# Kernel optimization log

Hardware: AMD Instinct MI355X
Metric: run time of the kernel (lower is better)

## Reference

```python
import jax, jax.numpy as jnp
import numpy as np

BEAM = 64
RANK = 32
VOCAB = 21128


def setup_inputs() -> dict:
    key = jax.random.key(0)
    k1, k2, k3, k4 = jax.random.split(key, 4)
    B, S, V = 16, 256, VOCAB
    emissions = jax.random.normal(k1, (B, S, V), jnp.float32)
    targets = jax.random.randint(k2, (B, S), 0, V)
    mask = jnp.ones((B, S), dtype=bool)
    E1 = jax.random.normal(k3, (V, RANK), jnp.float32) * 0.02
    E2 = jax.random.normal(k4, (V, RANK), jnp.float32) * 0.02
    return {"emissions": emissions, "targets": targets, "mask": mask, "E1": E1, "E2": E2}


def _crf_llh(emissions, targets, mask, E1, E2, beam=BEAM):
    B, S, V = emissions.shape
    maskf = mask.astype(emissions.dtype)

    # ---- numerator: score of the target path ----
    em = jnp.take_along_axis(emissions, targets[:, :, None], axis=2)[:, :, 0]  # [B,S]
    trans = jnp.sum(E1[targets[:, :-1]] * E2[targets[:, 1:]], axis=2)          # [B,S-1]
    scores = em.at[:, 1:].add(trans)
    numerator = jnp.sum(scores * maskf, axis=1)                                # [B]

    # ---- denominator: beam-approximated normalizer ----
    # force target token into the beam (scatter +inf, then topk indices)
    b_idx = jnp.arange(B)[:, None]
    s_idx = jnp.arange(S)[None, :]
    _em = emissions.at[b_idx, s_idx, targets].set(jnp.inf)
    _, beam_targets = jax.lax.top_k(_em, beam)                                 # [B,S,beam]
    beam_em = jnp.take_along_axis(emissions, beam_targets, axis=2)             # [B,S,beam]

    t1 = E1[beam_targets[:, :-1]]                                              # [B,S-1,beam,rank]
    t2 = E2[beam_targets[:, 1:]]                                               # [B,S-1,beam,rank]
    beam_trans = jnp.einsum('bsir,bsjr->bsij', t1, t2)                         # [B,S-1,beam,beam]

    score0 = beam_em[:, 0]                                                     # [B,beam]

    def step(score, x):
        trans_i, emit_i, m_i = x
        nxt = jax.scipy.special.logsumexp(score[:, :, None] + trans_i, axis=1) + emit_i
        score = jnp.where(m_i[:, None], nxt, score)
        return score, None

    xs = (jnp.swapaxes(beam_trans, 0, 1),          # [S-1,B,beam,beam]
          jnp.swapaxes(beam_em[:, 1:], 0, 1),      # [S-1,B,beam]
          jnp.swapaxes(mask[:, 1:], 0, 1))         # [S-1,B]
    score, _ = jax.lax.scan(step, score0, xs)
    denominator = jax.scipy.special.logsumexp(score, axis=1)                   # [B]

    llh = numerator - denominator
    return jnp.sum(llh)  # reduction='sum'


def reference(emissions, targets, mask, E1, E2):
    return _crf_llh(emissions, targets, mask, E1, E2)
```

## Files before the change

kernel.cpp:

```cpp
#include <hip/hip_runtime.h>
#include <stdint.h>

#define Bn 16
#define Sn 256
#define Vn 21128
#define NV4 5282
#define RANKn 32
#define BEAMn 64
#define HBINS 4096
#define CAPn 512
#define LOG2E 1.44269504088896340736f
#define LN2   0.69314718055994530942f

#define EXP2F(x) __builtin_amdgcn_exp2f(x)
#define LOG2F(x) __builtin_amdgcn_logf(x)

__device__ __forceinline__ unsigned f2o(unsigned b) {
    return (b & 0x80000000u) ? ~b : (b | 0x80000000u);
}
__device__ __forceinline__ float o2f(unsigned u) {
    unsigned b = (u & 0x80000000u) ? (u ^ 0x80000000u) : ~u;
    return __uint_as_float(b);
}
__device__ __forceinline__ float rdlane(float v, int lane) {
    return __int_as_float(__builtin_amdgcn_readlane(__float_as_int(v), lane));
}

__global__ __launch_bounds__(256) void topk_kernel(const float* __restrict__ emis,
                                                   const int* __restrict__ targets,
                                                   int* __restrict__ beam_idx,
                                                   float* __restrict__ beam_val) {
    const int row = blockIdx.x;
    const float* __restrict__ rowp = emis + (size_t)row * Vn;
    const int tgt = targets[row];
    __shared__ unsigned hist[HBINS];
    __shared__ unsigned csum[256];
    __shared__ unsigned cu[CAPn];
    __shared__ int      cix[CAPn];
    __shared__ int      selidx[BEAMn];
    __shared__ float    selval[BEAMn];
    __shared__ unsigned ccount;
    __shared__ int      binstar;
    __shared__ int      chunkc;
    __shared__ int      hastgt;
    const int t = threadIdx.x;
    for (int i = t; i < HBINS; i += 256) hist[i] = 0;
    if (t == 0) { ccount = 0; hastgt = 0; }
    __syncthreads();
    uint4 vals[21];
    #pragma unroll
    for (int it = 0; it < 21; ++it) {
        int v4 = t + it * 256;
        if (v4 < NV4) {
            const uint4 raw = ((const uint4*)rowp)[v4];
            uint4 u;
            u.x = f2o(raw.x); u.y = f2o(raw.y); u.z = f2o(raw.z); u.w = f2o(raw.w);
            vals[it] = u;
            atomicAdd(&hist[u.x >> 20], 1u);
            atomicAdd(&hist[u.y >> 20], 1u);
            atomicAdd(&hist[u.z >> 20], 1u);
            atomicAdd(&hist[u.w >> 20], 1u);
        }
    }
    __syncthreads();
    unsigned cs = 0;
    #pragma unroll
    for (int i = 0; i < 16; ++i) cs += hist[t * 16 + i];
    csum[t] = cs;
    __syncthreads();
    for (int off = 1; off < 256; off <<= 1) {
        unsigned v = csum[t] + ((t + off < 256) ? csum[t + off] : 0u);
        __syncthreads();
        csum[t] = v;
        __syncthreads();
    }
    if (csum[t] >= BEAMn && (t == 255 || csum[t + 1] < BEAMn)) chunkc = t;
    __syncthreads();
    if (t == 0) {
        int tc = chunkc;
        unsigned acc = (tc == 255) ? 0u : csum[tc + 1];
        int bs = tc * 16;
        for (int b2 = tc * 16 + 15; b2 >= tc * 16; --b2) {
            acc += hist[b2];
            if (acc >= BEAMn) { bs = b2; break; }
        }
        binstar = bs;
    }
    __syncthreads();
    const unsigned bstar = (unsigned)binstar;
    #pragma unroll
    for (int it = 0; it < 21; ++it) {
        int v4 = t + it * 256;
        if (v4 < NV4) {
            uint4 u = vals[it];
            int bi = v4 * 4;
            if ((u.x >> 20) >= bstar) { unsigned p = atomicAdd(&ccount, 1u); if (p < CAPn) { cu[p] = u.x; cix[p] = bi;     } }
            if ((u.y >> 20) >= bstar) { unsigned p = atomicAdd(&ccount, 1u); if (p < CAPn) { cu[p] = u.y; cix[p] = bi + 1; } }
            if ((u.z >> 20) >= bstar) { unsigned p = atomicAdd(&ccount, 1u); if (p < CAPn) { cu[p] = u.z; cix[p] = bi + 2; } }
            if ((u.w >> 20) >= bstar) { unsigned p = atomicAdd(&ccount, 1u); if (p < CAPn) { cu[p] = u.w; cix[p] = bi + 3; } }
        }
    }
    __syncthreads();
    const int C = (int)min(ccount, (unsigned)CAPn);
    for (int p = t; p < C; p += 256) {
        unsigned up = cu[p]; int ip = cix[p];
        int rank = 0;
        for (int q = 0; q < C; ++q) {
            unsigned uq = cu[q];
            rank += (uq > up) || (uq == up && cix[q] < ip);
        }
        if (rank < BEAMn) { selidx[rank] = ip; selval[rank] = o2f(up); }
    }
    __syncthreads();
    if (t < BEAMn && selidx[t] == tgt) hastgt = 1;
    __syncthreads();
    if (t == 0 && !hastgt) { selidx[BEAMn - 1] = tgt; selval[BEAMn - 1] = rowp[tgt]; }
    __syncthreads();
    if (t < BEAMn) {
        beam_idx[(size_t)row * BEAMn + t] = selidx[t];
        beam_val[(size_t)row * BEAMn + t] = selval[t];
    }
}

#define TPAD 68
__global__ __launch_bounds__(256) void trans_kernel(const float* __restrict__ E1,
                                                    const float* __restrict__ E2,
                                                    const int* __restrict__ beam_idx,
                                                    float* __restrict__ trans) {
    const int blk = blockIdx.x;
    const int b = blk / (Sn - 1);
    const int k = blk - b * (Sn - 1);
    const int* bi = beam_idx + ((size_t)(b * Sn + k)) * BEAMn;
    const int* bj = beam_idx + ((size_t)(b * Sn + k + 1)) * BEAMn;
    __shared__ float e1t[RANKn][TPAD];
    __shared__ float e2t[RANKn][TPAD];
    const int t = threadIdx.x;
    {
        const int row = t >> 2, q = t & 3;
        const int rb = q * 8;
        int i1 = bi[row];
        const float4* s1 = (const float4*)(E1 + (size_t)i1 * RANKn) + q * 2;
        float4 a0 = s1[0], a1 = s1[1];
        e1t[rb + 0][row] = a0.x; e1t[rb + 1][row] = a0.y; e1t[rb + 2][row] = a0.z; e1t[rb + 3][row] = a0.w;
        e1t[rb + 4][row] = a1.x; e1t[rb + 5][row] = a1.y; e1t[rb + 6][row] = a1.z; e1t[rb + 7][row] = a1.w;
        int i2 = bj[row];
        const float4* s2 = (const float4*)(E2 + (size_t)i2 * RANKn) + q * 2;
        float4 b0 = s2[0], b1 = s2[1];
        e2t[rb + 0][row] = b0.x; e2t[rb + 1][row] = b0.y; e2t[rb + 2][row] = b0.z; e2t[rb + 3][row] = b0.w;
        e2t[rb + 4][row] = b1.x; e2t[rb + 5][row] = b1.y; e2t[rb + 6][row] = b1.z; e2t[rb + 7][row] = b1.w;
    }
    __syncthreads();
    const int ti = t & 15, tj = t >> 4;
    const int i0 = ti * 4, j0 = tj * 4;
    float acc[4][4] = {};
    #pragma unroll
    for (int r = 0; r < RANKn; ++r) {
        float4 a = *(const float4*)&e1t[r][i0];
        float4 bb = *(const float4*)&e2t[r][j0];
        acc[0][0] += a.x * bb.x; acc[0][1] += a.x * bb.y; acc[0][2] += a.x * bb.z; acc[0][3] += a.x * bb.w;
        acc[1][0] += a.y * bb.x; acc[1][1] += a.y * bb.y; acc[1][2] += a.y * bb.z; acc[1][3] += a.y * bb.w;
        acc[2][0] += a.z * bb.x; acc[2][1] += a.z * bb.y; acc[2][2] += a.z * bb.z; acc[2][3] += a.z * bb.w;
        acc[3][0] += a.w * bb.x; acc[3][1] += a.w * bb.y; acc[3][2] += a.w * bb.z; acc[3][3] += a.w * bb.w;
    }
    float* outp = trans + (size_t)blk * (BEAMn * BEAMn);
    #pragma unroll
    for (int ii = 0; ii < 4; ++ii) {
        float4 o = { EXP2F(acc[ii][0] * LOG2E), EXP2F(acc[ii][1] * LOG2E),
                     EXP2F(acc[ii][2] * LOG2E), EXP2F(acc[ii][3] * LOG2E) };
        *(float4*)&outp[(i0 + ii) * BEAMn + j0] = o;
    }
}

__global__ __launch_bounds__(512) void scan_kernel(const float* __restrict__ trans,
                                                   const float* __restrict__ beam_val,
                                                   const int* __restrict__ mask,
                                                   float* __restrict__ out) {
    const int b = blockIdx.x;
    const int t = threadIdx.x;
    const int c = t >> 6, j = t & 63;
    const float* __restrict__ trb = trans + (size_t)b * (Sn - 1) * (BEAMn * BEAMn);
    const float* __restrict__ bv  = beam_val + (size_t)b * Sn * BEAMn;
    const int* __restrict__ mk = mask + (size_t)b * Sn;
    __shared__ float psum[2][8][BEAMn + 1];

    const unsigned long long mb0 = __ballot(mk[j] != 0);
    const unsigned long long mb1 = __ballot(mk[64 + j] != 0);
    const unsigned long long mb2 = __ballot(mk[128 + j] != 0);
    const unsigned long long mb3 = __ballot(mk[192 + j] != 0);

    float score_reg = bv[j] * LOG2E;
    float tba[8], tbb[8], tbc[8];
    float eba, ebb, ebc;
    const float* tp0 = trb + (c * 8) * BEAMn + j;
    #pragma unroll
    for (int r = 0; r < 8; ++r) tba[r] = tp0[r * BEAMn];
    #pragma unroll
    for (int r = 0; r < 8; ++r) tbb[r] = tp0[4096 + r * BEAMn];
    eba = bv[BEAMn + j] * LOG2E;
    ebb = bv[2 * BEAMn + j] * LOG2E;
    ebc = 0.f;

#define SSTEP(K, TA, EA, TC, EC)  {                                           \
    if ((K) + 2 < Sn - 1) {                                                   \
        const float* tpn = tp0 + (size_t)((K) + 2) * 4096;                    \
        _Pragma("unroll")                                                     \
        for (int r = 0; r < 8; ++r) TC[r] = tpn[r * BEAMn];                   \
        EC = bv[(size_t)((K) + 3) * BEAMn + j] * LOG2E;                       \
    }                                                                         \
    const float mt = rdlane(score_reg, 0);                                    \
    const float pj = EXP2F(score_reg - mt);                                   \
    float acc;                                                                \
    acc  = rdlane(pj, c * 8 + 0) * TA[0];                                     \
    acc += rdlane(pj, c * 8 + 1) * TA[1];                                     \
    acc += rdlane(pj, c * 8 + 2) * TA[2];                                     \
    acc += rdlane(pj, c * 8 + 3) * TA[3];                                     \
    acc += rdlane(pj, c * 8 + 4) * TA[4];                                     \
    acc += rdlane(pj, c * 8 + 5) * TA[5];                                     \
    acc += rdlane(pj, c * 8 + 6) * TA[6];                                     \
    acc += rdlane(pj, c * 8 + 7) * TA[7];                                     \
    psum[(K) & 1][c][j] = acc;                                                \
    __asm__ volatile("s_waitcnt lgkmcnt(0)\n\ts_barrier" ::: "memory");       \
    {                                                                         \
        const float (*ps)[BEAMn + 1] = psum[(K) & 1];                         \
        float tot = ps[0][j] + ps[1][j] + ps[2][j] + ps[3][j]                 \
                  + ps[4][j] + ps[5][j] + ps[6][j] + ps[7][j];                \
        float nxt = mt + LOG2F(tot) + EA;                                     \
        const int kk1 = (K) + 1;                                              \
        const unsigned long long bsel =                                       \
            (kk1 < 64) ? mb0 : (kk1 < 128) ? mb1 : (kk1 < 192) ? mb2 : mb3;  \
        score_reg = ((bsel >> (kk1 & 63)) & 1ull) ? nxt : score_reg;          \
    }                                                                         \
}

    for (int kb = 0; kb < Sn - 1; kb += 3) {
        SSTEP(kb,     tba, eba, tbc, ebc);
        SSTEP(kb + 1, tbb, ebb, tba, eba);
        SSTEP(kb + 2, tbc, ebc, tbb, ebb);
    }
#undef SSTEP

    if (t < BEAMn) {
        float v = score_reg;
        for (int off = 32; off; off >>= 1) v = fmaxf(v, __shfl_xor(v, off, 64));
        float e = EXP2F(score_reg - v);
        for (int off = 32; off; off >>= 1) e += __shfl_xor(e, off, 64);
        if (t == 0) atomicAdd(out, -LN2 * (v + LOG2F(e)));
    }
}

__global__ __launch_bounds__(256) void num_kernel(const float* __restrict__ emis,
                                                  const int* __restrict__ targets,
                                                  const int* __restrict__ mask,
                                                  const float* __restrict__ E1,
                                                  const float* __restrict__ E2,
                                                  float* __restrict__ out) {
    const int gid = blockIdx.x * 256 + threadIdx.x;
    float val = 0.f;
    if (gid < Bn * Sn) {
        int s = gid & (Sn - 1);
        int tg = targets[gid];
        float em = emis[(size_t)gid * Vn + tg];
        float tr = 0.f;
        if (s > 0) {
            int pv = targets[gid - 1];
            const float4* p1 = (const float4*)(E1 + (size_t)pv * RANKn);
            const float4* p2 = (const float4*)(E2 + (size_t)tg * RANKn);
            #pragma unroll
            for (int r = 0; r < 8; ++r) {
                float4 a = p1[r], bb = p2[r];
                tr += a.x * bb.x + a.y * bb.y + a.z * bb.z + a.w * bb.w;
            }
        }
        if (mask[gid]) val = em + tr;
    }
    for (int off = 32; off; off >>= 1) val += __shfl_xor(val, off, 64);
    __shared__ float wsum[4];
    if ((threadIdx.x & 63) == 0) wsum[threadIdx.x >> 6] = val;
    __syncthreads();
    if (threadIdx.x == 0) atomicAdd(out, wsum[0] + wsum[1] + wsum[2] + wsum[3]);
}

extern "C" void kernel_launch(void* const* d_in, const int* in_sizes, int n_in,
                              void* d_out, int out_size, void* d_ws, size_t ws_size,
                              hipStream_t stream) {
    const float* emis    = (const float*)d_in[0];
    const int*   targets = (const int*)d_in[1];
    const int*   mask    = (const int*)d_in[2];
    const float* E1      = (const float*)d_in[3];
    const float* E2      = (const float*)d_in[4];
    float* out = (float*)d_out;
    char* ws = (char*)d_ws;
    int*   beam_idx = (int*)ws;
    float* beam_val = (float*)(ws + (1 << 20));
    float* trans    = (float*)(ws + (2 << 20));

    (void)hipMemsetAsync(out, 0, sizeof(float), stream);
    hipLaunchKernelGGL(topk_kernel, dim3(Bn * Sn), dim3(256), 0, stream,
                       emis, targets, beam_idx, beam_val);
    hipLaunchKernelGGL(trans_kernel, dim3(Bn * (Sn - 1)), dim3(256), 0, stream,
                       E1, E2, beam_idx, trans);
    hipLaunchKernelGGL(num_kernel, dim3((Bn * Sn + 255) / 256), dim3(256), 0, stream,
                       emis, targets, mask, E1, E2, out);
    hipLaunchKernelGGL(scan_kernel, dim3(Bn), dim3(512), 0, stream,
                       trans, beam_val, mask, out);
}
```

Baseline: 679.0 us.

## Parallelize forward scan via segmented matrix products and add threshold fast path for top-k

The sequential 255-step logsumexp scan, which ran on only 16 blocks, is replaced by a segmented approach. 256 blocks each multiply 16 exp-domain transition matrices (with max-normalization tracked as a log scale), and a small finale kernel chains the 16 segment products per batch. Separately, top-k first tries a fixed value threshold (2.5) to collect candidates directly, skipping the histogram and prefix-scan passes when the count lands between 64 and 512, and falls back to the histogram otherwise. This trades far more arithmetic (64x64 matmuls) for much more parallelism, and adds exp-domain precision risk from rescaling by the max.

```diff
diff --git a/kernel.cpp b/kernel.cpp
--- a/kernel.cpp
+++ b/kernel.cpp
@@ -9,6 +9,7 @@
 #define BEAMn 64
 #define HBINS 4096
 #define CAPn 512
+#define NSEG 16
 #define LOG2E 1.44269504088896340736f
 #define LN2   0.69314718055994530942f
 
@@ -22,8 +23,8 @@
     unsigned b = (u & 0x80000000u) ? (u ^ 0x80000000u) : ~u;
     return __uint_as_float(b);
 }
-__device__ __forceinline__ float rdlane(float v, int lane) {
-    return __int_as_float(__builtin_amdgcn_readlane(__float_as_int(v), lane));
+__device__ __forceinline__ float dot4(float4 a, float4 b) {
+    return a.x * b.x + a.y * b.y + a.z * b.z + a.w * b.w;
 }
 
 __global__ __launch_bounds__(256) void topk_kernel(const float* __restrict__ emis,
@@ -43,11 +44,13 @@
     __shared__ int      binstar;
     __shared__ int      chunkc;
     __shared__ int      hastgt;
+    __shared__ unsigned wcnt[4];
     const int t = threadIdx.x;
-    for (int i = t; i < HBINS; i += 256) hist[i] = 0;
     if (t == 0) { ccount = 0; hastgt = 0; }
-    __syncthreads();
+
+    const unsigned THRU = f2o(__float_as_uint(2.5f));
     uint4 vals[21];
+    unsigned cntl = 0;
     #pragma unroll
     for (int it = 0; it < 21; ++it) {
         int v4 = t + it * 256;
@@ -56,48 +59,78 @@
             uint4 u;
             u.x = f2o(raw.x); u.y = f2o(raw.y); u.z = f2o(raw.z); u.w = f2o(raw.w);
             vals[it] = u;
-            atomicAdd(&hist[u.x >> 20], 1u);
-            atomicAdd(&hist[u.y >> 20], 1u);
-            atomicAdd(&hist[u.z >> 20], 1u);
-            atomicAdd(&hist[u.w >> 20], 1u);
-        }
-    }
-    __syncthreads();
-    unsigned cs = 0;
-    #pragma unroll
-    for (int i = 0; i < 16; ++i) cs += hist[t * 16 + i];
-    csum[t] = cs;
-    __syncthreads();
-    for (int off = 1; off < 256; off <<= 1) {
-        unsigned v = csum[t] + ((t + off < 256) ? csum[t + off] : 0u);
-        __syncthreads();
-        csum[t] = v;
-        __syncthreads();
-    }
-    if (csum[t] >= BEAMn && (t == 255 || csum[t + 1] < BEAMn)) chunkc = t;
-    __syncthreads();
-    if (t == 0) {
-        int tc = chunkc;
-        unsigned acc = (tc == 255) ? 0u : csum[tc + 1];
-        int bs = tc * 16;
-        for (int b2 = tc * 16 + 15; b2 >= tc * 16; --b2) {
-            acc += hist[b2];
-            if (acc >= BEAMn) { bs = b2; break; }
-        }
-        binstar = bs;
-    }
-    __syncthreads();
-    const unsigned bstar = (unsigned)binstar;
-    #pragma unroll
-    for (int it = 0; it < 21; ++it) {
-        int v4 = t + it * 256;
-        if (v4 < NV4) {
-            uint4 u = vals[it];
-            int bi = v4 * 4;
-            if ((u.x >> 20) >= bstar) { unsigned p = atomicAdd(&ccount, 1u); if (p < CAPn) { cu[p] = u.x; cix[p] = bi;     } }
-            if ((u.y >> 20) >= bstar) { unsigned p = atomicAdd(&ccount, 1u); if (p < CAPn) { cu[p] = u.y; cix[p] = bi + 1; } }
-            if ((u.z >> 20) >= bstar) { unsigned p = atomicAdd(&ccount, 1u); if (p < CAPn) { cu[p] = u.z; cix[p] = bi + 2; } }
-            if ((u.w >> 20) >= bstar) { unsigned p = atomicAdd(&ccount, 1u); if (p < CAPn) { cu[p] = u.w; cix[p] = bi + 3; } }
+            cntl += (u.x > THRU) + (u.y > THRU) + (u.z > THRU) + (u.w > THRU);
+        }
+    }
+    for (int off = 32; off; off >>= 1) cntl += __shfl_xor(cntl, off, 64);
+    if ((t & 63) == 0) wcnt[t >> 6] = cntl;
+    __syncthreads();
+    const unsigned C0 = wcnt[0] + wcnt[1] + wcnt[2] + wcnt[3];
+
+    if (C0 >= BEAMn && C0 <= CAPn) {
+        #pragma unroll
+        for (int it = 0; it < 21; ++it) {
+            int v4 = t + it * 256;
+            if (v4 < NV4) {
+                uint4 u = vals[it];
+                int bi = v4 * 4;
+                if (u.x > THRU) { unsigned p = atomicAdd(&ccount, 1u); cu[p] = u.x; cix[p] = bi;     }
+                if (u.y > THRU) { unsigned p = atomicAdd(&ccount, 1u); cu[p] = u.y; cix[p] = bi + 1; }
+                if (u.z > THRU) { unsigned p = atomicAdd(&ccount, 1u); cu[p] = u.z; cix[p] = bi + 2; }
+                if (u.w > THRU) { unsigned p = atomicAdd(&ccount, 1u); cu[p] = u.w; cix[p] = bi + 3; }
+            }
+        }
+    } else {
+        for (int i = t; i < HBINS; i += 256) hist[i] = 0;
+        __syncthreads();
+        #pragma unroll
+        for (int it = 0; it < 21; ++it) {
+            int v4 = t + it * 256;
+            if (v4 < NV4) {
+                uint4 u = vals[it];
+                atomicAdd(&hist[u.x >> 20], 1u);
+                atomicAdd(&hist[u.y >> 20], 1u);
+                atomicAdd(&hist[u.z >> 20], 1u);
+                atomicAdd(&hist[u.w >> 20], 1u);
+            }
+        }
+        __syncthreads();
+        unsigned cs = 0;
+        #pragma unroll
+        for (int i = 0; i < 16; ++i) cs += hist[t * 16 + i];
+        csum[t] = cs;
+        __syncthreads();
+        for (int off = 1; off < 256; off <<= 1) {
+            unsigned v = csum[t] + ((t + off < 256) ? csum[t + off] : 0u);
+            __syncthreads();
+            csum[t] = v;
+            __syncthreads();
+        }
+        if (csum[t] >= BEAMn && (t == 255 || csum[t + 1] < BEAMn)) chunkc = t;
+        __syncthreads();
+        if (t == 0) {
+            int tc = chunkc;
+            unsigned acc = (tc == 255) ? 0u : csum[tc + 1];
+            int bs = tc * 16;
+            for (int b2 = tc * 16 + 15; b2 >= tc * 16; --b2) {
+                acc += hist[b2];
+                if (acc >= BEAMn) { bs = b2; break; }
+            }
+            binstar = bs;
+        }
+        __syncthreads();
+        const unsigned bstar = (unsigned)binstar;
+        #pragma unroll
+        for (int it = 0; it < 21; ++it) {
+            int v4 = t + it * 256;
+            if (v4 < NV4) {
+                uint4 u = vals[it];
+                int bi = v4 * 4;
+                if ((u.x >> 20) >= bstar) { unsigned p = atomicAdd(&ccount, 1u); if (p < CAPn) { cu[p] = u.x; cix[p] = bi;     } }
+                if ((u.y >> 20) >= bstar) { unsigned p = atomicAdd(&ccount, 1u); if (p < CAPn) { cu[p] = u.y; cix[p] = bi + 1; } }
+                if ((u.z >> 20) >= bstar) { unsigned p = atomicAdd(&ccount, 1u); if (p < CAPn) { cu[p] = u.z; cix[p] = bi + 2; } }
+                if ((u.w >> 20) >= bstar) { unsigned p = atomicAdd(&ccount, 1u); if (p < CAPn) { cu[p] = u.w; cix[p] = bi + 3; } }
+            }
         }
     }
     __syncthreads();
@@ -171,80 +204,131 @@
     }
 }
 
-__global__ __launch_bounds__(512) void scan_kernel(const float* __restrict__ trans,
-                                                   const float* __restrict__ beam_val,
-                                                   const int* __restrict__ mask,
-                                                   float* __restrict__ out) {
+__global__ __launch_bounds__(256) void segprod_kernel(const float* __restrict__ trans,
+                                                      const float* __restrict__ beam_val,
+                                                      const int* __restrict__ mask,
+                                                      float* __restrict__ segP,
+                                                      float* __restrict__ segL) {
+    const int blk = blockIdx.x;
+    const int b = blk >> 4, s = blk & 15;
+    const int k0 = s * 16;
+    const int nk = min(16, (Sn - 1) - k0);
+    const float* __restrict__ trb = trans + ((size_t)b * (Sn - 1) + k0) * (BEAMn * BEAMn);
+    const float* __restrict__ bv  = beam_val + (size_t)b * Sn * BEAMn;
+    const int* __restrict__ mk = mask + (size_t)b * Sn;
+    __shared__ float Qa[64][64], Qb[64][64], Mld[64][64];
+    __shared__ float ev[16][64];
+    __shared__ int   mvec[16];
+    __shared__ float wmax[4];
+    const int t = threadIdx.x;
+    const int ti = t & 15, tj = t >> 4;
+    const int i0 = ti * 4, j0 = tj * 4;
+
+    for (int x = t; x < 4096; x += 256)
+        (&Qa[0][0])[x] = ((x >> 6) == (x & 63)) ? 1.f : 0.f;
+    for (int x = t; x < nk * 64; x += 256)
+        ev[x >> 6][x & 63] = EXP2F(bv[(size_t)(k0 + (x >> 6) + 1) * BEAMn + (x & 63)] * LOG2E);
+    if (t < nk) mvec[t] = mk[k0 + t + 1];
+    __syncthreads();
+
+    float (*Qc)[64] = Qa, (*Qn)[64] = Qb;
+    float L = 0.f;
+    for (int kk = 0; kk < nk; ++kk) {
+        const float4* Ms = (const float4*)(trb + (size_t)kk * (BEAMn * BEAMn));
+        #pragma unroll
+        for (int q = 0; q < 4; ++q) {
+            int p = t + q * 256;
+            int r = p >> 4, cc = (p & 15) * 4;
+            float4 v = Ms[p];
+            float4 e = *(const float4*)&ev[kk][cc];
+            v.x *= e.x; v.y *= e.y; v.z *= e.z; v.w *= e.w;
+            *(float4*)&Mld[r][cc] = v;
+        }
+        __syncthreads();
+        const int live = mvec[kk];
+        float acc[4][4];
+        if (live) {
+            #pragma unroll
+            for (int ii = 0; ii < 4; ++ii)
+                #pragma unroll
+                for (int jj = 0; jj < 4; ++jj) acc[ii][jj] = 0.f;
+            for (int r = 0; r < 64; ++r) {
+                float4 a  = *(const float4*)&Qc[r][i0];
+                float4 bb = *(const float4*)&Mld[r][j0];
+                acc[0][0] += a.x * bb.x; acc[0][1] += a.x * bb.y; acc[0][2] += a.x * bb.z; acc[0][3] += a.x * bb.w;
+                acc[1][0] += a.y * bb.x; acc[1][1] += a.y * bb.y; acc[1][2] += a.y * bb.z; acc[1][3] += a.y * bb.w;
+                acc[2][0] += a.z * bb.x; acc[2][1] += a.z * bb.y; acc[2][2] += a.z * bb.z; acc[2][3] += a.z * bb.w;
+                acc[3][0] += a.w * bb.x; acc[3][1] += a.w * bb.y; acc[3][2] += a.w * bb.z; acc[3][3] += a.w * bb.w;
+            }
+            float lm = acc[0][0];
+            #pragma unroll
+            for (int ii = 0; ii < 4; ++ii)
+                #pragma unroll
+                for (int jj = 0; jj < 4; ++jj) lm = fmaxf(lm, acc[ii][jj]);
+            for (int off = 32; off; off >>= 1) lm = fmaxf(lm, __shfl_xor(lm, off, 64));
+            if ((t & 63) == 0) wmax[t >> 6] = lm;
+        }
+        __syncthreads();
+        if (live) {
+            const float m = fmaxf(fmaxf(wmax[0], wmax[1]), fmaxf(wmax[2], wmax[3]));
+            const float inv = 1.f / m;
+            #pragma unroll
+            for (int jj = 0; jj < 4; ++jj) {
+                float4 w = { acc[0][jj] * inv, acc[1][jj] * inv, acc[2][jj] * inv, acc[3][jj] * inv };
+                *(float4*)&Qn[j0 + jj][i0] = w;
+            }
+            L += LOG2F(m);
+            float (*tmp)[64] = Qc; Qc = Qn; Qn = tmp;
+        }
+        __syncthreads();
+    }
+    float* op = segP + (size_t)blk * 4096;
+    for (int x = t; x < 4096; x += 256) op[x] = (&Qc[0][0])[x];
+    if (t == 0) segL[blk] = L;
+}
+
+__global__ __launch_bounds__(256) void finale_kernel(const float* __restrict__ segP,
+                                                     const float* __restrict__ segL,
+                                                     const float* __restrict__ beam_val,
+                                                     float* __restrict__ out) {
     const int b = blockIdx.x;
     const int t = threadIdx.x;
-    const int c = t >> 6, j = t & 63;
-    const float* __restrict__ trb = trans + (size_t)b * (Sn - 1) * (BEAMn * BEAMn);
-    const float* __restrict__ bv  = beam_val + (size_t)b * Sn * BEAMn;
-    const int* __restrict__ mk = mask + (size_t)b * Sn;
-    __shared__ float psum[2][8][BEAMn + 1];
-
-    const unsigned long long mb0 = __ballot(mk[j] != 0);
-    const unsigned long long mb1 = __ballot(mk[64 + j] != 0);
-    const unsigned long long mb2 = __ballot(mk[128 + j] != 0);
-    const unsigned long long mb3 = __ballot(mk[192 + j] != 0);
-
-    float score_reg = bv[j] * LOG2E;
-    float tba[8], tbb[8], tbc[8];
-    float eba, ebb, ebc;
-    const float* tp0 = trb + (c * 8) * BEAMn + j;
-    #pragma unroll
-    for (int r = 0; r < 8; ++r) tba[r] = tp0[r * BEAMn];
-    #pragma unroll
-    for (int r = 0; r < 8; ++r) tbb[r] = tp0[4096 + r * BEAMn];
-    eba = bv[BEAMn + j] * LOG2E;
-    ebb = bv[2 * BEAMn + j] * LOG2E;
-    ebc = 0.f;
-
-#define SSTEP(K, TA, EA, TC, EC)  {                                           \
-    if ((K) + 2 < Sn - 1) {                                                   \
-        const float* tpn = tp0 + (size_t)((K) + 2) * 4096;                    \
-        _Pragma("unroll")                                                     \
-        for (int r = 0; r < 8; ++r) TC[r] = tpn[r * BEAMn];                   \
-        EC = bv[(size_t)((K) + 3) * BEAMn + j] * LOG2E;                       \
-    }                                                                         \
-    const float mt = rdlane(score_reg, 0);                                    \
-    const float pj = EXP2F(score_reg - mt);                                   \
-    float acc;                                                                \
-    acc  = rdlane(pj, c * 8 + 0) * TA[0];                                     \
-    acc += rdlane(pj, c * 8 + 1) * TA[1];                                     \
-    acc += rdlane(pj, c * 8 + 2) * TA[2];                                     \
-    acc += rdlane(pj, c * 8 + 3) * TA[3];                                     \
-    acc += rdlane(pj, c * 8 + 4) * TA[4];                                     \
-    acc += rdlane(pj, c * 8 + 5) * TA[5];                                     \
-    acc += rdlane(pj, c * 8 + 6) * TA[6];                                     \
-    acc += rdlane(pj, c * 8 + 7) * TA[7];                                     \
-    psum[(K) & 1][c][j] = acc;                                                \
-    __asm__ volatile("s_waitcnt lgkmcnt(0)\n\ts_barrier" ::: "memory");       \
-    {                                                                         \
-        const float (*ps)[BEAMn + 1] = psum[(K) & 1];                         \
-        float tot = ps[0][j] + ps[1][j] + ps[2][j] + ps[3][j]                 \
-                  + ps[4][j] + ps[5][j] + ps[6][j] + ps[7][j];                \
-        float nxt = mt + LOG2F(tot) + EA;                                     \
-        const int kk1 = (K) + 1;                                              \
-        const unsigned long long bsel =                                       \
-            (kk1 < 64) ? mb0 : (kk1 < 128) ? mb1 : (kk1 < 192) ? mb2 : mb3;  \
-        score_reg = ((bsel >> (kk1 & 63)) & 1ull) ? nxt : score_reg;          \
-    }                                                                         \
-}
-
-    for (int kb = 0; kb < Sn - 1; kb += 3) {
-        SSTEP(kb,     tba, eba, tbc, ebc);
-        SSTEP(kb + 1, tbb, ebb, tba, eba);
-        SSTEP(kb + 2, tbc, ebc, tbb, ebb);
-    }
-#undef SSTEP
-
+    const int w = t >> 6, j = t & 63;
+    const float* __restrict__ bv = beam_val + (size_t)b * Sn * BEAMn;
+    __shared__ float us[BEAMn];
+    __shared__ float part[4][BEAMn + 1];
+    float sc = bv[j] * LOG2E;
+    float mx = sc;
+    for (int off = 32; off; off >>= 1) mx = fmaxf(mx, __shfl_xor(mx, off, 64));
+    float u = EXP2F(sc - mx);
+    float Ltot = mx;
+    const float* p0 = segP + ((size_t)b * NSEG) * 4096 + (size_t)j * 64 + w * 16;
+    float4 ra0 = ((const float4*)p0)[0], ra1 = ((const float4*)p0)[1],
+           ra2 = ((const float4*)p0)[2], ra3 = ((const float4*)p0)[3];
+    for (int s2 = 0; s2 < NSEG; ++s2) {
+        float4 rb0, rb1, rb2, rb3;
+        if (s2 + 1 < NSEG) {
+            const float* pn = segP + ((size_t)b * NSEG + s2 + 1) * 4096 + (size_t)j * 64 + w * 16;
+            rb0 = ((const float4*)pn)[0]; rb1 = ((const float4*)pn)[1];
+            rb2 = ((const float4*)pn)[2]; rb3 = ((const float4*)pn)[3];
+        }
+        if (w == 0) us[j] = u;
+        __syncthreads();
+        const float4* uu = (const float4*)&us[w * 16];
+        float a2 = dot4(ra0, uu[0]) + dot4(ra1, uu[1]) + dot4(ra2, uu[2]) + dot4(ra3, uu[3]);
+        part[w][j] = a2;
+        __syncthreads();
+        float tot = part[0][j] + part[1][j] + part[2][j] + part[3][j];
+        float m = tot;
+        for (int off = 32; off; off >>= 1) m = fmaxf(m, __shfl_xor(m, off, 64));
+        u = tot / m;
+        Ltot += LOG2F(m) + segL[b * NSEG + s2];
+        ra0 = rb0; ra1 = rb1; ra2 = rb2; ra3 = rb3;
+    }
     if (t < BEAMn) {
-        float v = score_reg;
-        for (int off = 32; off; off >>= 1) v = fmaxf(v, __shfl_xor(v, off, 64));
-        float e = EXP2F(score_reg - v);
+        float e = u;
         for (int off = 32; off; off >>= 1) e += __shfl_xor(e, off, 64);
-        if (t == 0) atomicAdd(out, -LN2 * (v + LOG2F(e)));
+        if (t == 0) atomicAdd(out, -LN2 * (Ltot + LOG2F(e)));
     }
 }
 
@@ -293,6 +377,8 @@
     int*   beam_idx = (int*)ws;
     float* beam_val = (float*)(ws + (1 << 20));
     float* trans    = (float*)(ws + (2 << 20));
+    float* segP     = (float*)(ws + ((size_t)69 << 20));
+    float* segL     = (float*)(ws + ((size_t)74 << 20));
 
     (void)hipMemsetAsync(out, 0, sizeof(float), stream);
     hipLaunchKernelGGL(topk_kernel, dim3(Bn * Sn), dim3(256), 0, stream,
@@ -301,6 +387,8 @@
                        E1, E2, beam_idx, trans);
     hipLaunchKernelGGL(num_kernel, dim3((Bn * Sn + 255) / 256), dim3(256), 0, stream,
                        emis, targets, mask, E1, E2, out);
-    hipLaunchKernelGGL(scan_kernel, dim3(Bn), dim3(512), 0, stream,
-                       trans, beam_val, mask, out);
-}
+    hipLaunchKernelGGL(segprod_kernel, dim3(Bn * NSEG), dim3(256), 0, stream,
+                       trans, beam_val, mask, segP, segL);
+    hipLaunchKernelGGL(finale_kernel, dim3(Bn), dim3(256), 0, stream,
+                       segP, segL, beam_val, out);
+}
```

After: 573.5 us. 1.18x faster.
